# Kernel tuning notes

Hardware: AMD Instinct MI355X
Metric: run time of the kernel (lower is better)

## Reference

```python
import jax, jax.numpy as jnp
import numpy as np

B, S, D = 1, 2048, 2048
H = 16
HD = D // H           # 128
FFN_H = 5632          # int(2*4*D/3) rounded up to multiple of 256
EPS = 1e-5
ROPE_THETA = 10000.0


def rms_norm(x, w, eps=EPS):
    # x * rsqrt(mean(x^2, -1) + eps) * w
    return x * jax.lax.rsqrt(jnp.mean(x * x, axis=-1, keepdims=True) + eps) * w


def apply_rope(x, cos, sin):
    # x: [B, S, H, HD]; cos/sin: [S, HD//2]
    b, s, h, hd = x.shape
    xr = x.reshape(b, s, h, hd // 2, 2)
    x_re, x_im = xr[..., 0], xr[..., 1]
    c = cos[None, :, None, :]
    sn = sin[None, :, None, :]
    o_re = x_re * c - x_im * sn
    o_im = x_re * sn + x_im * c
    return jnp.stack([o_re, o_im], axis=-1).reshape(b, s, h, hd)


def setup_inputs() -> dict:
    key = jax.random.key(0)
    ks = jax.random.split(key, 10)
    x = jax.random.normal(ks[0], (B, S, D), dtype=jnp.float32)
    # RoPE frequencies (Llama-style)
    inv_freq = 1.0 / (ROPE_THETA ** (np.arange(0, HD, 2, dtype=np.float32) / HD))
    angles = np.outer(np.arange(S, dtype=np.float32), inv_freq)  # [S, HD//2]
    freqs_cos = jnp.asarray(np.cos(angles), dtype=jnp.float32)
    freqs_sin = jnp.asarray(np.sin(angles), dtype=jnp.float32)
    # causal mask: 1 = keep, 0 = masked
    mask = jnp.tril(jnp.ones((S, S), dtype=jnp.int32))[None, None]
    sc = 0.02
    return {
        "x": x,
        "freqs_cos": freqs_cos,
        "freqs_sin": freqs_sin,
        "mask": mask,
        "wq": jax.random.normal(ks[1], (D, D), jnp.float32) * sc,
        "wk": jax.random.normal(ks[2], (D, D), jnp.float32) * sc,
        "wv": jax.random.normal(ks[3], (D, D), jnp.float32) * sc,
        "wo": jax.random.normal(ks[4], (D, D), jnp.float32) * sc,
        "w1": jax.random.normal(ks[5], (D, FFN_H), jnp.float32) * sc,
        "w2": jax.random.normal(ks[6], (FFN_H, D), jnp.float32) * sc,
        "w3": jax.random.normal(ks[7], (D, FFN_H), jnp.float32) * sc,
        "attn_norm_w": jnp.ones((D,), jnp.float32),
        "ffn_norm_w": jnp.ones((D,), jnp.float32),
    }


def reference(x, freqs_cos, freqs_sin, mask, wq, wk, wv, wo, w1, w2, w3,
              attn_norm_w, ffn_norm_w):
    b, s, d = x.shape
    # --- attention block ---
    xn = rms_norm(x, attn_norm_w)
    q = (xn @ wq).reshape(b, s, H, HD)
    k = (xn @ wk).reshape(b, s, H, HD)
    v = (xn @ wv).reshape(b, s, H, HD)
    q = apply_rope(q, freqs_cos, freqs_sin)
    k = apply_rope(k, freqs_cos, freqs_sin)
    scores = jnp.einsum('bqhd,bkhd->bhqk', q, k) / jnp.sqrt(jnp.float32(HD))
    scores = jnp.where(mask == 0, -jnp.inf, scores)
    probs = jax.nn.softmax(scores, axis=-1)
    attn = jnp.einsum('bhqk,bkhd->bqhd', probs, v).reshape(b, s, d)
    h = x + attn @ wo
    # --- SwiGLU FFN block ---
    hn = rms_norm(h, ffn_norm_w)
    ff = (jax.nn.silu(hn @ w1) * (hn @ w3)) @ w2
    return h + ff
```

## Files before the change

kernel.cpp:

```cpp
#include <hip/hip_runtime.h>
#include <hip/hip_bf16.h>

typedef __bf16 bf16x8 __attribute__((ext_vector_type(8)));
typedef float f32x4 __attribute__((ext_vector_type(4)));
typedef unsigned short u16x8 __attribute__((ext_vector_type(8)));
typedef unsigned short u16x4 __attribute__((ext_vector_type(4)));

#define DEV static __device__ __forceinline__

DEV unsigned short f2bf(float f) {
    unsigned u = __builtin_bit_cast(unsigned, f);
    u += 0x7fffu + ((u >> 16) & 1u);
    return (unsigned short)(u >> 16);
}
DEV float bf2f(unsigned short h) {
    unsigned u = ((unsigned)h) << 16;
    return __builtin_bit_cast(float, u);
}

DEV void gl2lds16(const void* g, void* l) {
    __builtin_amdgcn_global_load_lds(
        (const __attribute__((address_space(1))) void*)g,
        (__attribute__((address_space(3))) void*)l, 16, 0, 0);
}

#define WAITV(N) asm volatile("s_waitcnt vmcnt(" #N ")" ::: "memory")
#define SBAR()   asm volatile("s_barrier" ::: "memory")

#define STAGE256(KT, SLOT, BUF)                                               \
    {                                                                         \
        const unsigned short* sbase = ((SLOT) & 1)                            \
            ? BT + (size_t)(bn + ((SLOT) >> 1) * 128) * K                     \
            : A  + (size_t)(bm + ((SLOT) >> 1) * 128) * K;                    \
        _Pragma("unroll")                                                     \
        for (int j = 0; j < 2; ++j) {                                         \
            const unsigned short* g = sbase + (size_t)(srow + j * 64) * K     \
                                      + (KT) * 64 + lc;                       \
            gl2lds16(g, &lds[BUF][SLOT][wave * 512 + j * 4096]);              \
        }                                                                     \
    }

#define COMPUTE256(BUF, MH, NH)                                               \
    {                                                                         \
        const char* Ab = (const char*)&lds[BUF][(MH) * 2][0];                 \
        const char* Bb = (const char*)&lds[BUF][(NH) * 2 + 1][0];             \
        bf16x8 a_[4][2], b_[2][2];                                            \
        _Pragma("unroll")                                                     \
        for (int m4 = 0; m4 < 4; ++m4) {                                      \
            _Pragma("unroll")                                                 \
            for (int kk = 0; kk < 2; ++kk)                                    \
                a_[m4][kk] = *(const bf16x8*)(Ab +                            \
                    (wm * 64 + m4 * 16 + lr) * 128 +                          \
                    ((kk * 64 + lg * 16) ^ xsw));                             \
        }                                                                     \
        _Pragma("unroll")                                                     \
        for (int n2 = 0; n2 < 2; ++n2) {                                      \
            _Pragma("unroll")                                                 \
            for (int kk = 0; kk < 2; ++kk)                                    \
                b_[n2][kk] = *(const bf16x8*)(Bb +                            \
                    (wn * 32 + n2 * 16 + lr) * 128 +                          \
                    ((kk * 64 + lg * 16) ^ xsw));                             \
        }                                                                     \
        __builtin_amdgcn_s_setprio(1);                                        \
        _Pragma("unroll")                                                     \
        for (int m4 = 0; m4 < 4; ++m4)                                        \
            _Pragma("unroll")                                                 \
            for (int n2 = 0; n2 < 2; ++n2)                                    \
                _Pragma("unroll")                                             \
                for (int kk = 0; kk < 2; ++kk)                                \
                    acc[(MH) * 4 + m4][(NH) * 2 + n2] =                       \
                        __builtin_amdgcn_mfma_f32_16x16x32_bf16(              \
                            a_[m4][kk], b_[n2][kk],                           \
                            acc[(MH) * 4 + m4][(NH) * 2 + n2], 0, 0, 0);      \
        __builtin_amdgcn_s_setprio(0);                                        \
    }

__global__ __launch_bounds__(512, 2)
void gemm256_bt(const unsigned short* __restrict__ A,
                const unsigned short* __restrict__ BT,
                unsigned short* __restrict__ outB,
                int M, int N, int K)
{
    __shared__ alignas(16) unsigned short lds[2][4][8192];
    const int tid  = threadIdx.x;
    const int lane = tid & 63;
    const int wave = tid >> 6;
    const int wm = wave >> 2;
    const int wn = wave & 3;
    const int lr = lane & 15;
    const int lg = lane >> 4;
    const int lin = blockIdx.y * gridDim.x + blockIdx.x;
    const int cpx = (gridDim.x * gridDim.y) >> 3;
    const int swz = (lin & 7) * cpx + (lin >> 3);
    const int bm = (swz & 7) * 256;
    const int bn = (swz >> 3) * 256;
    const int xsw  = (lr & 7) << 4;
    const int srow = tid >> 3;
    const int lc   = ((tid & 7) ^ (srow & 7)) * 8;

    f32x4 acc[8][4] = {};
    const int NT = K >> 6;

    STAGE256(0, 0, 0); STAGE256(0, 1, 0); STAGE256(0, 2, 0); STAGE256(0, 3, 0);
    for (int kt = 0; kt < NT - 1; ++kt) {
        const int buf = kt & 1, nbuf = buf ^ 1;
        STAGE256(kt + 1, 0, nbuf);
        WAITV(6); SBAR();
        COMPUTE256(buf, 0, 0);
        STAGE256(kt + 1, 1, nbuf);
        WAITV(6); SBAR();
        COMPUTE256(buf, 1, 0);
        STAGE256(kt + 1, 2, nbuf);
        WAITV(6); SBAR();
        COMPUTE256(buf, 1, 1);
        STAGE256(kt + 1, 3, nbuf);
        COMPUTE256(buf, 0, 1);
        SBAR();
    }
    {
        const int buf = (NT - 1) & 1;
        WAITV(4); SBAR();
        COMPUTE256(buf, 0, 0);
        WAITV(2); SBAR();
        COMPUTE256(buf, 1, 0);
        WAITV(0); SBAR();
        COMPUTE256(buf, 1, 1);
        COMPUTE256(buf, 0, 1);
    }

#pragma unroll
    for (int m = 0; m < 8; ++m) {
        const int row = bm + (m >> 2) * 128 + wm * 64 + (m & 3) * 16 + lg * 4;
#pragma unroll
        for (int n = 0; n < 4; ++n) {
            const int col = bn + (n >> 1) * 128 + wn * 32 + (n & 1) * 16 + lr;
#pragma unroll
            for (int r = 0; r < 4; ++r)
                outB[(size_t)(row + r) * N + col] = f2bf(acc[m][n][r]);
        }
    }
}

#define STAGE128(KT, SLOT, BUF)                                               \
    {                                                                         \
        const unsigned short* sbase = ((SLOT) == 0)                           \
            ? A  + (size_t)bm * K                                             \
            : BT + (size_t)(bn + ((SLOT) - 1) * 128) * K;                     \
        _Pragma("unroll")                                                     \
        for (int j = 0; j < 2; ++j) {                                         \
            const unsigned short* g = sbase + (size_t)(srow + j * 64) * K     \
                                      + koff + (KT) * 64 + lc;                \
            gl2lds16(g, &lds[BUF][SLOT][wave * 512 + j * 4096]);              \
        }                                                                     \
    }

#define COMPUTE128(BUF, KK)                                                   \
    {                                                                         \
        const char* Ab = (const char*)&lds[BUF][0][0];                        \
        const char* Bb = (const char*)&lds[BUF][1 + (wn >> 1)][0];            \
        bf16x8 a_[4], b_[4];                                                  \
        _Pragma("unroll")                                                     \
        for (int m4 = 0; m4 < 4; ++m4)                                        \
            a_[m4] = *(const bf16x8*)(Ab + (wm * 64 + m4 * 16 + lr) * 128 +   \
                     (((KK) * 64 + lg * 16) ^ xsw));                          \
        _Pragma("unroll")                                                     \
        for (int n2 = 0; n2 < 4; ++n2)                                        \
            b_[n2] = *(const bf16x8*)(Bb +                                    \
                     ((wn & 1) * 64 + n2 * 16 + lr) * 128 +                   \
                     (((KK) * 64 + lg * 16) ^ xsw));                          \
        __builtin_amdgcn_s_setprio(1);                                        \
        _Pragma("unroll")                                                     \
        for (int m4 = 0; m4 < 4; ++m4)                                        \
            _Pragma("unroll")                                                 \
            for (int n2 = 0; n2 < 4; ++n2)                                    \
                acc[m4][n2] = __builtin_amdgcn_mfma_f32_16x16x32_bf16(        \
                    a_[m4], b_[n2], acc[m4][n2], 0, 0, 0);                    \
        __builtin_amdgcn_s_setprio(0);                                        \
    }

template <bool SPLITK>
__global__ __launch_bounds__(512, 2)
void gemm128_bt(const unsigned short* __restrict__ A,
                const unsigned short* __restrict__ BT,
                unsigned short* __restrict__ outB,
                float* __restrict__ outP,
                int M, int N, int K)
{
    __shared__ alignas(16) unsigned short lds[2][3][8192];
    const int tid  = threadIdx.x;
    const int lane = tid & 63;
    const int wave = tid >> 6;
    const int wm = wave >> 2;
    const int wn = wave & 3;
    const int lr = lane & 15;
    const int lg = lane >> 4;
    const int gy  = gridDim.y;
    const int lin = blockIdx.y * gridDim.x + blockIdx.x;
    const int cpx = (gridDim.x * gy) >> 3;
    const int swz = (lin & 7) * cpx + (lin >> 3);
    const int bm = (swz % gy) * 128;
    const int bn = (swz / gy) * 256;
    const int xsw  = (lr & 7) << 4;
    const int srow = tid >> 3;
    const int lc   = ((tid & 7) ^ (srow & 7)) * 8;
    int koff, NT;
    if constexpr (SPLITK) { const int Kh = K >> 1; koff = blockIdx.z * Kh; NT = Kh >> 6; }
    else                  { koff = 0;              NT = K >> 6; }

    f32x4 acc[4][4] = {};

    STAGE128(0, 0, 0); STAGE128(0, 1, 0); STAGE128(0, 2, 0);
    for (int kt = 0; kt < NT - 1; ++kt) {
        const int buf = kt & 1, nbuf = buf ^ 1;
        STAGE128(kt + 1, 0, nbuf);
        STAGE128(kt + 1, 1, nbuf);
        WAITV(4); SBAR();
        COMPUTE128(buf, 0);
        STAGE128(kt + 1, 2, nbuf);
        COMPUTE128(buf, 1);
        SBAR();
    }
    {
        const int buf = (NT - 1) & 1;
        WAITV(0); SBAR();
        COMPUTE128(buf, 0);
        COMPUTE128(buf, 1);
    }

#pragma unroll
    for (int m4 = 0; m4 < 4; ++m4) {
        const int row = bm + wm * 64 + m4 * 16 + lg * 4;
#pragma unroll
        for (int n2 = 0; n2 < 4; ++n2) {
            const int col = bn + wn * 64 + n2 * 16 + lr;
#pragma unroll
            for (int r = 0; r < 4; ++r) {
                if constexpr (SPLITK)
                    outP[(size_t)blockIdx.z * M * N + (size_t)(row + r) * N + col] = acc[m4][n2][r];
                else
                    outB[(size_t)(row + r) * N + col] = f2bf(acc[m4][n2][r]);
            }
        }
    }
}

__global__ __launch_bounds__(256)
void reduce2_add(const float* res, const float* p, float* out, int n4)
{
    const float4* r4 = (const float4*)res;
    const float4* a4 = (const float4*)p;
    const float4* b4 = (const float4*)(p + (size_t)2048 * 2048);
    float4* o4 = (float4*)out;
    for (int i = blockIdx.x * 256 + threadIdx.x; i < n4; i += gridDim.x * 256) {
        const float4 r = r4[i], a = a4[i], b = b4[i];
        o4[i] = make_float4(r.x + a.x + b.x, r.y + a.y + b.y,
                            r.z + a.z + b.z, r.w + a.w + b.w);
    }
}

__global__ __launch_bounds__(256)
void reduce2_norm(const float* __restrict__ res, const float* __restrict__ p,
                  const float* __restrict__ w, float* __restrict__ hout,
                  unsigned short* __restrict__ nout)
{
    const int row = blockIdx.x, tid = threadIdx.x;
    const float4* r4 = (const float4*)(res + (size_t)row * 2048);
    const float4* a4 = (const float4*)(p   + (size_t)row * 2048);
    const float4* b4 = (const float4*)(p + (size_t)2048 * 2048 + (size_t)row * 2048);
    float4* h4 = (float4*)(hout + (size_t)row * 2048);
    float4 h[2];
    float ss = 0.f;
#pragma unroll
    for (int i = 0; i < 2; ++i) {
        const int idx = i * 256 + tid;
        const float4 r = r4[idx], a = a4[idx], b = b4[idx];
        float4 v = make_float4(r.x + a.x + b.x, r.y + a.y + b.y,
                               r.z + a.z + b.z, r.w + a.w + b.w);
        h[i] = v; h4[idx] = v;
        ss += v.x * v.x + v.y * v.y + v.z * v.z + v.w * v.w;
    }
#pragma unroll
    for (int off = 32; off; off >>= 1) ss += __shfl_xor(ss, off);
    __shared__ float red[4];
    if ((tid & 63) == 0) red[tid >> 6] = ss;
    __syncthreads();
    const float tot = red[0] + red[1] + red[2] + red[3];
    const float sc = rsqrtf(tot * (1.0f / 2048.0f) + 1e-5f);
#pragma unroll
    for (int i = 0; i < 2; ++i) {
        const int idx = i * 256 + tid;
        const float4 wv = ((const float4*)w)[idx];
        u16x4 o;
        o[0] = f2bf(h[i].x * sc * wv.x); o[1] = f2bf(h[i].y * sc * wv.y);
        o[2] = f2bf(h[i].z * sc * wv.z); o[3] = f2bf(h[i].w * sc * wv.w);
        *(u16x4*)(nout + (size_t)row * 2048 + idx * 4) = o;
    }
}

__global__ __launch_bounds__(256)
void rmsnorm_kernel(const float* __restrict__ x, const float* __restrict__ w,
                    unsigned short* __restrict__ out)
{
    const int row = blockIdx.x;
    const int tid = threadIdx.x;
    const float* xr = x + (size_t)row * 2048;
    const float4 a = *reinterpret_cast<const float4*>(xr + tid * 8);
    const float4 b = *reinterpret_cast<const float4*>(xr + tid * 8 + 4);
    float ss = a.x * a.x + a.y * a.y + a.z * a.z + a.w * a.w
             + b.x * b.x + b.y * b.y + b.z * b.z + b.w * b.w;
#pragma unroll
    for (int off = 32; off; off >>= 1) ss += __shfl_xor(ss, off);
    __shared__ float red[4];
    if ((tid & 63) == 0) red[tid >> 6] = ss;
    __syncthreads();
    const float tot = red[0] + red[1] + red[2] + red[3];
    const float sc = rsqrtf(tot * (1.0f / 2048.0f) + 1e-5f);
    const float4 wa = *reinterpret_cast<const float4*>(w + tid * 8);
    const float4 wb = *reinterpret_cast<const float4*>(w + tid * 8 + 4);
    u16x8 o;
    o[0] = f2bf(a.x * sc * wa.x); o[1] = f2bf(a.y * sc * wa.y);
    o[2] = f2bf(a.z * sc * wa.z); o[3] = f2bf(a.w * sc * wa.w);
    o[4] = f2bf(b.x * sc * wb.x); o[5] = f2bf(b.y * sc * wb.y);
    o[6] = f2bf(b.z * sc * wb.z); o[7] = f2bf(b.w * sc * wb.w);
    *reinterpret_cast<u16x8*>(out + (size_t)row * 2048 + tid * 8) = o;
}

__global__ __launch_bounds__(256)
void rope_kernel(unsigned short* __restrict__ t, const float* __restrict__ cs,
                 const float* __restrict__ sn)
{
    const int idx = blockIdx.x * 256 + threadIdx.x;
    const int s   = idx >> 9;
    const int col = (idx & 511) * 8;
    const int i0  = (col & 127) >> 1;
    u16x8 v = *reinterpret_cast<const u16x8*>(t + (size_t)s * 6144 + col);
    const float4 c  = *reinterpret_cast<const float4*>(cs + s * 64 + i0);
    const float4 sv = *reinterpret_cast<const float4*>(sn + s * 64 + i0);
    const float cc[4] = {c.x, c.y, c.z, c.w};
    const float ns[4] = {sv.x, sv.y, sv.z, sv.w};
#pragma unroll
    for (int p = 0; p < 4; ++p) {
        const float re = bf2f(v[2 * p]), im = bf2f(v[2 * p + 1]);
        v[2 * p]     = f2bf(re * cc[p] - im * ns[p]);
        v[2 * p + 1] = f2bf(re * ns[p] + im * cc[p]);
    }
    *reinterpret_cast<u16x8*>(t + (size_t)s * 6144 + col) = v;
}

__global__ __launch_bounds__(256)
void transpose_bf16(const unsigned short* __restrict__ in,
                    unsigned short* __restrict__ out, int M, int N, int ldin)
{
    __shared__ unsigned short t[64][66];
    const int bm = blockIdx.y * 64, bn = blockIdx.x * 64;
    const int tid = threadIdx.x;
    const int r = tid >> 3, c8 = (tid & 7) * 8;
#pragma unroll
    for (int i = 0; i < 2; ++i) {
        const int row = r + i * 32;
        u16x8 v = *reinterpret_cast<const u16x8*>(in + (size_t)(bm + row) * ldin + bn + c8);
#pragma unroll
        for (int e = 0; e < 8; ++e) t[row][c8 + e] = v[e];
    }
    __syncthreads();
#pragma unroll
    for (int i = 0; i < 2; ++i) {
        const int orow = r + i * 32;
        u16x8 v;
#pragma unroll
        for (int e = 0; e < 8; ++e) v[e] = t[c8 + e][orow];
        *reinterpret_cast<u16x8*>(out + (size_t)(bn + orow) * M + bm + c8) = v;
    }
}

__global__ __launch_bounds__(256)
void convT_kernel(const float* __restrict__ w, unsigned short* __restrict__ wT,
                  int K, int N)
{
    __shared__ unsigned short t[64][66];
    const int bk = blockIdx.y * 64, bn = blockIdx.x * 64;
    const int tid = threadIdx.x;
    const int r = tid >> 4, c4 = (tid & 15) * 4;
#pragma unroll
    for (int i = 0; i < 4; ++i) {
        const int row = r + i * 16;
        const float4 v = *reinterpret_cast<const float4*>(w + (size_t)(bk + row) * N + bn + c4);
        t[row][c4 + 0] = f2bf(v.x); t[row][c4 + 1] = f2bf(v.y);
        t[row][c4 + 2] = f2bf(v.z); t[row][c4 + 3] = f2bf(v.w);
    }
    __syncthreads();
#pragma unroll
    for (int i = 0; i < 4; ++i) {
        const int n = r + i * 16;
        u16x4 o;
#pragma unroll
        for (int e = 0; e < 4; ++e) o[e] = t[c4 + e][n];
        *reinterpret_cast<u16x4*>(wT + (size_t)(bn + n) * K + bk + c4) = o;
    }
}

__global__ __launch_bounds__(256)
void silu_mul_kernel(const unsigned short* __restrict__ t13,
                     unsigned short* __restrict__ g)
{
    const int s  = blockIdx.y;
    const int c8 = (blockIdx.x * 256 + threadIdx.x) * 8;
    if (c8 >= 5632) return;
    const unsigned short* row = t13 + (size_t)s * 11264;
    const u16x8 va = *reinterpret_cast<const u16x8*>(row + c8);
    const u16x8 vb = *reinterpret_cast<const u16x8*>(row + 5632 + c8);
    u16x8 o;
#pragma unroll
    for (int e = 0; e < 8; ++e) {
        const float x = bf2f(va[e]);
        const float y = bf2f(vb[e]);
        const float sv = x / (1.0f + __expf(-x));
        o[e] = f2bf(sv * y);
    }
    *reinterpret_cast<u16x8*>(g + (size_t)s * 5632 + c8) = o;
}

__global__ __launch_bounds__(512)
void flash_attn(const unsigned short* __restrict__ q,
                const unsigned short* __restrict__ k,
                const unsigned short* __restrict__ vT,
                unsigned short* __restrict__ attn)
{
    __shared__ alignas(16) unsigned short Ks[2][64][136];
    __shared__ alignas(16) unsigned short Vs[2][128][72];
    __shared__ alignas(16) unsigned short Ps[8][16][72];

    const int hh = blockIdx.y;
    const int pi = blockIdx.x;
    const int tid = threadIdx.x;
    const int lane = tid & 63, wave = tid >> 6;
    const int qt = (wave >> 2) ? (31 - pi) : pi;
    const int lr = lane & 15, lg = lane >> 4;
    const int q0 = qt * 64 + (wave & 3) * 16;
    const int myNT = qt + 1;
    const int NT   = 32 - pi;

    const int kr0 = tid >> 4, kc0 = (tid & 15) * 8;
    const int vr0 = tid >> 3, vc0 = (tid & 7) * 8;

    bf16x8 qf[4];
#pragma unroll
    for (int c = 0; c < 4; ++c)
        qf[c] = *reinterpret_cast<const bf16x8*>(
            q + (size_t)(q0 + lr) * 6144 + hh * 128 + c * 32 + lg * 8);

    f32x4 oacc[8] = {};
    float m_r[4], l_r[4];
#pragma unroll
    for (int r = 0; r < 4; ++r) { m_r[r] = -INFINITY; l_r[r] = 0.0f; }
    const float scale = 0.08838834764831845f;

    u16x8 kreg0, kreg1, vreg0, vreg1;
    auto gload = [&](int kt) {
        const int kv0 = kt * 64;
        kreg0 = *reinterpret_cast<const u16x8*>(k + (size_t)(kv0 + kr0) * 6144 + hh * 128 + kc0);
        kreg1 = *reinterpret_cast<const u16x8*>(k + (size_t)(kv0 + kr0 + 32) * 6144 + hh * 128 + kc0);
        vreg0 = *reinterpret_cast<const u16x8*>(vT + (size_t)(hh * 128 + vr0) * 2048 + kv0 + vc0);
        vreg1 = *reinterpret_cast<const u16x8*>(vT + (size_t)(hh * 128 + vr0 + 64) * 2048 + kv0 + vc0);
    };
    auto lwrite = [&](int buf) {
        *reinterpret_cast<u16x8*>(&Ks[buf][kr0][kc0])      = kreg0;
        *reinterpret_cast<u16x8*>(&Ks[buf][kr0 + 32][kc0]) = kreg1;
        *reinterpret_cast<u16x8*>(&Vs[buf][vr0][vc0])      = vreg0;
        *reinterpret_cast<u16x8*>(&Vs[buf][vr0 + 64][vc0]) = vreg1;
    };

    gload(0); lwrite(0);
    __syncthreads();

    for (int kt = 0; kt < NT; ++kt) {
        const int buf = kt & 1;
        if (kt + 1 < NT) gload(kt + 1);

        if (kt < myNT) {
            const int kv0 = kt * 64;
            const bool masked = (kt == myNT - 1);
            f32x4 s[4] = {};
            __builtin_amdgcn_s_setprio(1);
#pragma unroll
            for (int ct = 0; ct < 4; ++ct)
#pragma unroll
                for (int c = 0; c < 4; ++c) {
                    const bf16x8 kf = *reinterpret_cast<const bf16x8*>(
                        &Ks[buf][ct * 16 + lr][c * 32 + lg * 8]);
                    s[ct] = __builtin_amdgcn_mfma_f32_16x16x32_bf16(qf[c], kf, s[ct], 0, 0, 0);
                }
            __builtin_amdgcn_s_setprio(0);
#pragma unroll
            for (int ct = 0; ct < 4; ++ct)
#pragma unroll
                for (int r = 0; r < 4; ++r) {
                    float v = s[ct][r] * scale;
                    if (masked) {
                        const int kvg = kv0 + ct * 16 + lr;
                        const int qg  = q0 + lg * 4 + r;
                        if (kvg > qg) v = -INFINITY;
                    }
                    s[ct][r] = v;
                }
            float mn[4], alpha[4], rs[4];
#pragma unroll
            for (int r = 0; r < 4; ++r) {
                float v = fmaxf(fmaxf(s[0][r], s[1][r]), fmaxf(s[2][r], s[3][r]));
                v = fmaxf(v, __shfl_xor(v, 1));
                v = fmaxf(v, __shfl_xor(v, 2));
                v = fmaxf(v, __shfl_xor(v, 4));
                v = fmaxf(v, __shfl_xor(v, 8));
                mn[r] = fmaxf(m_r[r], v);
                alpha[r] = __expf(m_r[r] - mn[r]);
                m_r[r] = mn[r];
                rs[r] = 0.0f;
            }
#pragma unroll
            for (int ct = 0; ct < 4; ++ct)
#pragma unroll
                for (int r = 0; r < 4; ++r) {
                    const float p = __expf(s[ct][r] - mn[r]);
                    s[ct][r] = p;
                    rs[r] += p;
                }
#pragma unroll
            for (int r = 0; r < 4; ++r) {
                float t2 = rs[r];
                t2 += __shfl_xor(t2, 1);
                t2 += __shfl_xor(t2, 2);
                t2 += __shfl_xor(t2, 4);
                t2 += __shfl_xor(t2, 8);
                l_r[r] = l_r[r] * alpha[r] + t2;
            }
#pragma unroll
            for (int ot = 0; ot < 8; ++ot)
#pragma unroll
                for (int r = 0; r < 4; ++r) oacc[ot][r] *= alpha[r];

#pragma unroll
            for (int ct = 0; ct < 4; ++ct)
#pragma unroll
                for (int r = 0; r < 4; ++r)
                    Ps[wave][lg * 4 + r][ct * 16 + lr] = f2bf(s[ct][r]);

            __builtin_amdgcn_s_setprio(1);
#pragma unroll
            for (int c2 = 0; c2 < 2; ++c2) {
                const bf16x8 pf = *reinterpret_cast<const bf16x8*>(
                    &Ps[wave][lr][c2 * 32 + lg * 8]);
#pragma unroll
                for (int ot = 0; ot < 8; ++ot) {
                    const bf16x8 vf = *reinterpret_cast<const bf16x8*>(
                        &Vs[buf][ot * 16 + lr][c2 * 32 + lg * 8]);
                    oacc[ot] = __builtin_amdgcn_mfma_f32_16x16x32_bf16(pf, vf, oacc[ot], 0, 0, 0);
                }
            }
            __builtin_amdgcn_s_setprio(0);
        }

        if (kt + 1 < NT) lwrite(buf ^ 1);
        __syncthreads();
    }

#pragma unroll
    for (int ot = 0; ot < 8; ++ot)
#pragma unroll
        for (int r = 0; r < 4; ++r) {
            const float v = oacc[ot][r] / l_r[r];
            attn[(size_t)(q0 + lg * 4 + r) * 2048 + hh * 128 + ot * 16 + lr] = f2bf(v);
        }
}

extern "C" void kernel_launch(void* const* d_in, const int* in_sizes, int n_in,
                              void* d_out, int out_size, void* d_ws, size_t ws_size,
                              hipStream_t stream)
{
    const float* x    = (const float*)d_in[0];
    const float* fcos = (const float*)d_in[1];
    const float* fsin = (const float*)d_in[2];
    const float* wq  = (const float*)d_in[4];
    const float* wk  = (const float*)d_in[5];
    const float* wv  = (const float*)d_in[6];
    const float* wo  = (const float*)d_in[7];
    const float* w1  = (const float*)d_in[8];
    const float* w2  = (const float*)d_in[9];
    const float* w3  = (const float*)d_in[10];
    const float* anw = (const float*)d_in[11];
    const float* fnw = (const float*)d_in[12];
    float* out = (float*)d_out;

    char* ws = (char*)d_ws;
    size_t off = 0;
    auto alloc = [&](size_t bytes) { void* p = ws + off; off += bytes; return p; };
    const size_t SZ_DD = (size_t)2048 * 2048 * 2;
    const size_t SZ_DF = (size_t)2048 * 5632 * 2;

    unsigned short* wqT = (unsigned short*)alloc(SZ_DD);
    unsigned short* wkT = (unsigned short*)alloc(SZ_DD);
    unsigned short* wvT = (unsigned short*)alloc(SZ_DD);
    unsigned short* woT = (unsigned short*)alloc(SZ_DD);
    unsigned short* w1T = (unsigned short*)alloc(SZ_DF);
    unsigned short* w3T = (unsigned short*)alloc(SZ_DF);
    unsigned short* w2T = (unsigned short*)alloc(SZ_DF);

    char* reg1 = (char*)alloc((size_t)48 * 1024 * 1024);
    unsigned short* xn   = (unsigned short*)reg1;
    unsigned short* qkv  = (unsigned short*)(reg1 + SZ_DD);
    unsigned short* vTb  = (unsigned short*)(reg1 + SZ_DD + 3 * SZ_DD);
    unsigned short* ab   = (unsigned short*)(reg1 + SZ_DD + 4 * SZ_DD);
    unsigned short* t13  = (unsigned short*)reg1;
    float*          pk   = (float*)reg1;

    char* reg2 = (char*)alloc(SZ_DF);
    unsigned short* hn = (unsigned short*)reg2;
    unsigned short* t1 = (unsigned short*)reg2;

    const int N4 = 2048 * 2048 / 4;

    convT_kernel<<<dim3(32, 32), 256, 0, stream>>>(wq, wqT, 2048, 2048);
    convT_kernel<<<dim3(32, 32), 256, 0, stream>>>(wk, wkT, 2048, 2048);
    convT_kernel<<<dim3(32, 32), 256, 0, stream>>>(wv, wvT, 2048, 2048);
    convT_kernel<<<dim3(32, 32), 256, 0, stream>>>(wo, woT, 2048, 2048);
    convT_kernel<<<dim3(88, 32), 256, 0, stream>>>(w1, w1T, 2048, 5632);
    convT_kernel<<<dim3(88, 32), 256, 0, stream>>>(w3, w3T, 2048, 5632);
    convT_kernel<<<dim3(32, 88), 256, 0, stream>>>(w2, w2T, 5632, 2048);

    rmsnorm_kernel<<<2048, 256, 0, stream>>>(x, anw, xn);
    gemm256_bt<<<dim3(24, 8), 512, 0, stream>>>(xn, wqT, qkv, 2048, 6144, 2048);
    rope_kernel<<<4096, 256, 0, stream>>>(qkv, fcos, fsin);
    transpose_bf16<<<dim3(32, 32), 256, 0, stream>>>(qkv + 4096, vTb, 2048, 2048, 6144);
    flash_attn<<<dim3(16, 16), 512, 0, stream>>>(qkv, qkv + 2048, vTb, ab);
    gemm128_bt<true><<<dim3(8, 16, 2), 512, 0, stream>>>(ab, woT, nullptr, pk, 2048, 2048, 2048);
    reduce2_norm<<<2048, 256, 0, stream>>>(x, pk, fnw, out, hn);

    gemm128_bt<false><<<dim3(44, 16), 512, 0, stream>>>(hn, w1T, t13, nullptr, 2048, 11264, 2048);
    silu_mul_kernel<<<dim3(3, 2048), 256, 0, stream>>>(t13, t1);
    gemm128_bt<true><<<dim3(8, 16, 2), 512, 0, stream>>>(t1, w2T, nullptr, pk, 2048, 2048, 5632);
    reduce2_add<<<2048, 256, 0, stream>>>(out, pk, out, N4);
}
```

Before: 450.6 us.

## Fuse SiLU-mul into W1/W3 GEMM epilogue and triple-buffer gemm128 pipeline

```diff
diff --git a/kernel.cpp b/kernel.cpp
--- a/kernel.cpp
+++ b/kernel.cpp
@@ -141,52 +141,60 @@
     }
 }
 
-#define STAGE128(KT, SLOT, BUF)                                               \
-    {                                                                         \
-        const unsigned short* sbase = ((SLOT) == 0)                           \
+#define STAGE128D(KT, BUF)                                                    \
+    _Pragma("unroll")                                                         \
+    for (int sl = 0; sl < 3; ++sl) {                                          \
+        const unsigned short* sbase = (sl == 0)                               \
             ? A  + (size_t)bm * K                                             \
-            : BT + (size_t)(bn + ((SLOT) - 1) * 128) * K;                     \
+            : BT + (size_t)(bn + (sl - 1) * 128) * K;                         \
         _Pragma("unroll")                                                     \
         for (int j = 0; j < 2; ++j) {                                         \
             const unsigned short* g = sbase + (size_t)(srow + j * 64) * K     \
                                       + koff + (KT) * 64 + lc;                \
-            gl2lds16(g, &lds[BUF][SLOT][wave * 512 + j * 4096]);              \
+            gl2lds16(g, &lds[BUF][sl][wave * 512 + j * 4096]);                \
         }                                                                     \
     }
 
-#define COMPUTE128(BUF, KK)                                                   \
+#define COMPUTE128D(BUF)                                                      \
     {                                                                         \
         const char* Ab = (const char*)&lds[BUF][0][0];                        \
         const char* Bb = (const char*)&lds[BUF][1 + (wn >> 1)][0];            \
-        bf16x8 a_[4], b_[4];                                                  \
+        bf16x8 a_[4][2], b_[4][2];                                            \
         _Pragma("unroll")                                                     \
         for (int m4 = 0; m4 < 4; ++m4)                                        \
-            a_[m4] = *(const bf16x8*)(Ab + (wm * 64 + m4 * 16 + lr) * 128 +   \
-                     (((KK) * 64 + lg * 16) ^ xsw));                          \
+            _Pragma("unroll")                                                 \
+            for (int kk = 0; kk < 2; ++kk)                                    \
+                a_[m4][kk] = *(const bf16x8*)(Ab +                            \
+                    (wm * 64 + m4 * 16 + lr) * 128 +                          \
+                    ((kk * 64 + lg * 16) ^ xsw));                             \
         _Pragma("unroll")                                                     \
         for (int n2 = 0; n2 < 4; ++n2)                                        \
-            b_[n2] = *(const bf16x8*)(Bb +                                    \
-                     ((wn & 1) * 64 + n2 * 16 + lr) * 128 +                   \
-                     (((KK) * 64 + lg * 16) ^ xsw));                          \
+            _Pragma("unroll")                                                 \
+            for (int kk = 0; kk < 2; ++kk)                                    \
+                b_[n2][kk] = *(const bf16x8*)(Bb +                            \
+                    ((wn & 1) * 64 + n2 * 16 + lr) * 128 +                    \
+                    ((kk * 64 + lg * 16) ^ xsw));                             \
         __builtin_amdgcn_s_setprio(1);                                        \
         _Pragma("unroll")                                                     \
         for (int m4 = 0; m4 < 4; ++m4)                                        \
             _Pragma("unroll")                                                 \
             for (int n2 = 0; n2 < 4; ++n2)                                    \
-                acc[m4][n2] = __builtin_amdgcn_mfma_f32_16x16x32_bf16(        \
-                    a_[m4], b_[n2], acc[m4][n2], 0, 0, 0);                    \
+                _Pragma("unroll")                                             \
+                for (int kk = 0; kk < 2; ++kk)                                \
+                    acc[m4][n2] = __builtin_amdgcn_mfma_f32_16x16x32_bf16(    \
+                        a_[m4][kk], b_[n2][kk], acc[m4][n2], 0, 0, 0);        \
         __builtin_amdgcn_s_setprio(0);                                        \
     }
 
-template <bool SPLITK>
+template <int EPI>
 __global__ __launch_bounds__(512, 2)
-void gemm128_bt(const unsigned short* __restrict__ A,
-                const unsigned short* __restrict__ BT,
-                unsigned short* __restrict__ outB,
-                float* __restrict__ outP,
-                int M, int N, int K)
-{
-    __shared__ alignas(16) unsigned short lds[2][3][8192];
+void gemm128d(const unsigned short* __restrict__ A,
+              const unsigned short* __restrict__ BT,
+              unsigned short* __restrict__ outB,
+              float* __restrict__ outP,
+              int M, int N, int K)
+{
+    __shared__ alignas(16) unsigned short lds[3][3][8192];
     const int tid  = threadIdx.x;
     const int lane = tid & 63;
     const int wave = tid >> 6;
@@ -204,28 +212,28 @@
     const int srow = tid >> 3;
     const int lc   = ((tid & 7) ^ (srow & 7)) * 8;
     int koff, NT;
-    if constexpr (SPLITK) { const int Kh = K >> 1; koff = blockIdx.z * Kh; NT = Kh >> 6; }
-    else                  { koff = 0;              NT = K >> 6; }
+    if constexpr (EPI == 1) { const int Kh = K >> 1; koff = blockIdx.z * Kh; NT = Kh >> 6; }
+    else                    { koff = 0;              NT = K >> 6; }
 
     f32x4 acc[4][4] = {};
 
-    STAGE128(0, 0, 0); STAGE128(0, 1, 0); STAGE128(0, 2, 0);
-    for (int kt = 0; kt < NT - 1; ++kt) {
-        const int buf = kt & 1, nbuf = buf ^ 1;
-        STAGE128(kt + 1, 0, nbuf);
-        STAGE128(kt + 1, 1, nbuf);
-        WAITV(4); SBAR();
-        COMPUTE128(buf, 0);
-        STAGE128(kt + 1, 2, nbuf);
-        COMPUTE128(buf, 1);
+    STAGE128D(0, 0);
+    STAGE128D(1, 1);
+    int bc = 0;
+    for (int kt = 0; kt + 2 < NT; ++kt) {
+        const int nb = (bc == 0) ? 2 : bc - 1;
+        STAGE128D(kt + 2, nb);
+        WAITV(12); SBAR();
+        COMPUTE128D(bc);
         SBAR();
-    }
-    {
-        const int buf = (NT - 1) & 1;
-        WAITV(0); SBAR();
-        COMPUTE128(buf, 0);
-        COMPUTE128(buf, 1);
-    }
+        bc = (bc == 2) ? 0 : bc + 1;
+    }
+    WAITV(6); SBAR();
+    COMPUTE128D(bc);
+    SBAR();
+    bc = (bc == 2) ? 0 : bc + 1;
+    WAITV(0); SBAR();
+    COMPUTE128D(bc);
 
 #pragma unroll
     for (int m4 = 0; m4 < 4; ++m4) {
@@ -235,10 +243,19 @@
             const int col = bn + wn * 64 + n2 * 16 + lr;
 #pragma unroll
             for (int r = 0; r < 4; ++r) {
-                if constexpr (SPLITK)
+                if constexpr (EPI == 0) {
+                    outB[(size_t)(row + r) * N + col] = f2bf(acc[m4][n2][r]);
+                } else if constexpr (EPI == 1) {
                     outP[(size_t)blockIdx.z * M * N + (size_t)(row + r) * N + col] = acc[m4][n2][r];
-                else
-                    outB[(size_t)(row + r) * N + col] = f2bf(acc[m4][n2][r]);
+                } else {
+                    const float v  = acc[m4][n2][r];
+                    const float vo = __shfl_xor(v, 1);
+                    const float x1 = (lr & 1) ? vo : v;
+                    const float x3 = (lr & 1) ? v : vo;
+                    const float g  = x1 / (1.0f + __expf(-x1)) * x3;
+                    if (!(lr & 1))
+                        outB[(size_t)(row + r) * (N >> 1) + (col >> 1)] = f2bf(g);
+                }
             }
         }
     }
@@ -375,7 +392,7 @@
 
 __global__ __launch_bounds__(256)
 void convT_kernel(const float* __restrict__ w, unsigned short* __restrict__ wT,
-                  int K, int N)
+                  int K, int N, int rmul, int radd)
 {
     __shared__ unsigned short t[64][66];
     const int bk = blockIdx.y * 64, bn = blockIdx.x * 64;
@@ -395,29 +412,8 @@
         u16x4 o;
 #pragma unroll
         for (int e = 0; e < 4; ++e) o[e] = t[c4 + e][n];
-        *reinterpret_cast<u16x4*>(wT + (size_t)(bn + n) * K + bk + c4) = o;
-    }
-}
-
-__global__ __launch_bounds__(256)
-void silu_mul_kernel(const unsigned short* __restrict__ t13,
-                     unsigned short* __restrict__ g)
-{
-    const int s  = blockIdx.y;
-    const int c8 = (blockIdx.x * 256 + threadIdx.x) * 8;
-    if (c8 >= 5632) return;
-    const unsigned short* row = t13 + (size_t)s * 11264;
-    const u16x8 va = *reinterpret_cast<const u16x8*>(row + c8);
-    const u16x8 vb = *reinterpret_cast<const u16x8*>(row + 5632 + c8);
-    u16x8 o;
-#pragma unroll
-    for (int e = 0; e < 8; ++e) {
-        const float x = bf2f(va[e]);
-        const float y = bf2f(vb[e]);
-        const float sv = x / (1.0f + __expf(-x));
-        o[e] = f2bf(sv * y);
-    }
-    *reinterpret_cast<u16x8*>(g + (size_t)s * 5632 + c8) = o;
+        *reinterpret_cast<u16x4*>(wT + (size_t)(rmul * (bn + n) + radd) * K + bk + c4) = o;
+    }
 }
 
 __global__ __launch_bounds__(512)
@@ -596,46 +592,43 @@
     const size_t SZ_DD = (size_t)2048 * 2048 * 2;
     const size_t SZ_DF = (size_t)2048 * 5632 * 2;
 
-    unsigned short* wqT = (unsigned short*)alloc(SZ_DD);
-    unsigned short* wkT = (unsigned short*)alloc(SZ_DD);
-    unsigned short* wvT = (unsigned short*)alloc(SZ_DD);
-    unsigned short* woT = (unsigned short*)alloc(SZ_DD);
-    unsigned short* w1T = (unsigned short*)alloc(SZ_DF);
-    unsigned short* w3T = (unsigned short*)alloc(SZ_DF);
-    unsigned short* w2T = (unsigned short*)alloc(SZ_DF);
+    unsigned short* wqT  = (unsigned short*)alloc(SZ_DD);
+    unsigned short* wkT  = (unsigned short*)alloc(SZ_DD);
+    unsigned short* wvT  = (unsigned short*)alloc(SZ_DD);
+    unsigned short* woT  = (unsigned short*)alloc(SZ_DD);
+    unsigned short* w13T = (unsigned short*)alloc(2 * SZ_DF);
+    unsigned short* w2T  = (unsigned short*)alloc(SZ_DF);
 
     char* reg1 = (char*)alloc((size_t)48 * 1024 * 1024);
     unsigned short* xn   = (unsigned short*)reg1;
     unsigned short* qkv  = (unsigned short*)(reg1 + SZ_DD);
     unsigned short* vTb  = (unsigned short*)(reg1 + SZ_DD + 3 * SZ_DD);
     unsigned short* ab   = (unsigned short*)(reg1 + SZ_DD + 4 * SZ_DD);
-    unsigned short* t13  = (unsigned short*)reg1;
     float*          pk   = (float*)reg1;
+    unsigned short* hn   = (unsigned short*)(reg1 + 4 * SZ_DD);
 
     char* reg2 = (char*)alloc(SZ_DF);
-    unsigned short* hn = (unsigned short*)reg2;
     unsigned short* t1 = (unsigned short*)reg2;
 
     const int N4 = 2048 * 2048 / 4;
 
-    convT_kernel<<<dim3(32, 32), 256, 0, stream>>>(wq, wqT, 2048, 2048);
-    convT_kernel<<<dim3(32, 32), 256, 0, stream>>>(wk, wkT, 2048, 2048);
-    convT_kernel<<<dim3(32, 32), 256, 0, stream>>>(wv, wvT, 2048, 2048);
-    convT_kernel<<<dim3(32, 32), 256, 0, stream>>>(wo, woT, 2048, 2048);
-    convT_kernel<<<dim3(88, 32), 256, 0, stream>>>(w1, w1T, 2048, 5632);
-    convT_kernel<<<dim3(88, 32), 256, 0, stream>>>(w3, w3T, 2048, 5632);
-    convT_kernel<<<dim3(32, 88), 256, 0, stream>>>(w2, w2T, 5632, 2048);
+    convT_kernel<<<dim3(32, 32), 256, 0, stream>>>(wq, wqT, 2048, 2048, 1, 0);
+    convT_kernel<<<dim3(32, 32), 256, 0, stream>>>(wk, wkT, 2048, 2048, 1, 0);
+    convT_kernel<<<dim3(32, 32), 256, 0, stream>>>(wv, wvT, 2048, 2048, 1, 0);
+    convT_kernel<<<dim3(32, 32), 256, 0, stream>>>(wo, woT, 2048, 2048, 1, 0);
+    convT_kernel<<<dim3(88, 32), 256, 0, stream>>>(w1, w13T, 2048, 5632, 2, 0);
+    convT_kernel<<<dim3(88, 32), 256, 0, stream>>>(w3, w13T, 2048, 5632, 2, 1);
+    convT_kernel<<<dim3(32, 88), 256, 0, stream>>>(w2, w2T, 5632, 2048, 1, 0);
 
     rmsnorm_kernel<<<2048, 256, 0, stream>>>(x, anw, xn);
     gemm256_bt<<<dim3(24, 8), 512, 0, stream>>>(xn, wqT, qkv, 2048, 6144, 2048);
     rope_kernel<<<4096, 256, 0, stream>>>(qkv, fcos, fsin);
     transpose_bf16<<<dim3(32, 32), 256, 0, stream>>>(qkv + 4096, vTb, 2048, 2048, 6144);
     flash_attn<<<dim3(16, 16), 512, 0, stream>>>(qkv, qkv + 2048, vTb, ab);
-    gemm128_bt<true><<<dim3(8, 16, 2), 512, 0, stream>>>(ab, woT, nullptr, pk, 2048, 2048, 2048);
+    gemm128d<1><<<dim3(8, 16, 2), 512, 0, stream>>>(ab, woT, nullptr, pk, 2048, 2048, 2048);
     reduce2_norm<<<2048, 256, 0, stream>>>(x, pk, fnw, out, hn);
 
-    gemm128_bt<false><<<dim3(44, 16), 512, 0, stream>>>(hn, w1T, t13, nullptr, 2048, 11264, 2048);
-    silu_mul_kernel<<<dim3(3, 2048), 256, 0, stream>>>(t13, t1);
-    gemm128_bt<true><<<dim3(8, 16, 2), 512, 0, stream>>>(t1, w2T, nullptr, pk, 2048, 2048, 5632);
+    gemm128d<2><<<dim3(44, 16), 512, 0, stream>>>(hn, w13T, t1, nullptr, 2048, 11264, 2048);
+    gemm128d<1><<<dim3(8, 16, 2), 512, 0, stream>>>(t1, w2T, nullptr, pk, 2048, 2048, 5632);
     reduce2_add<<<2048, 256, 0, stream>>>(out, pk, out, N4);
 }
```

Measured after the change: 439.3 us. 1.03x faster.
